# Kernel tuning notes

Measured on AMD Instinct MI355X. Metric: run time of the kernel, lower is better.

## Reference

```python
import jax, jax.numpy as jnp
import numpy as np
import math

IN_DIM = 256
HID_DIM = 256
NUM_EDGE_TYPES = 3
HEADS = 8
HEAD_DIM = HID_DIM // HEADS  # 32
QK_DIM = (NUM_EDGE_TYPES + 1) * HID_DIM  # 1024
N = 4096


def _glorot(key, shape):
    # torch_geometric-style glorot: uniform(-a, a), a = sqrt(6/(fan_in+fan_out)) over last two dims
    a = math.sqrt(6.0 / (shape[-2] + shape[-1]))
    return jax.random.uniform(key, shape, jnp.float32, -a, a)


def setup_inputs() -> dict:
    key = jax.random.key(0)
    ks = jax.random.split(key, 8)
    return {
        "input_x": jax.random.normal(ks[0], (N, IN_DIM), jnp.float32),
        "pe_Q": jax.random.normal(ks[1], (N, NUM_EDGE_TYPES * HID_DIM), jnp.float32),
        "pe_K": jax.random.normal(ks[2], (N, NUM_EDGE_TYPES * HID_DIM), jnp.float32),
        "A": jnp.zeros((N, N), jnp.int32),  # accepted by forward but unused
        "WQ": _glorot(ks[3], (HEADS, QK_DIM, HEAD_DIM)),
        "WK": _glorot(ks[4], (HEADS, QK_DIM, HEAD_DIM)),
        "WV": _glorot(ks[5], (HEADS, IN_DIM, HEAD_DIM)),
        "Q_bias": jnp.zeros((HEADS, 1, HEAD_DIM), jnp.float32),
        "K_bias": jnp.zeros((HEADS, 1, HEAD_DIM), jnp.float32),
        "V_bias": jnp.zeros((HEADS, 1, HEAD_DIM), jnp.float32),
        "lin_w": _glorot(ks[6], (HID_DIM, HID_DIM)),
        "lin_b": jnp.zeros((HID_DIM,), jnp.float32),
    }


def reference(input_x, pe_Q, pe_K, A, WQ, WK, WV, Q_bias, K_bias, V_bias, lin_w, lin_b):
    x_Q = jnp.concatenate([input_x, pe_Q], axis=-1)  # [N, QK_DIM]
    x_K = jnp.concatenate([input_x, pe_K], axis=-1)  # [N, QK_DIM]
    Q = jnp.einsum('nd,hdk->hnk', x_Q, WQ) + Q_bias   # [H, N, hd]
    K = jnp.einsum('nd,hdk->hnk', x_K, WK) + K_bias   # [H, N, hd]
    V = jnp.einsum('nd,hdk->hnk', input_x, WV) + V_bias
    scores = jnp.einsum('hnk,hmk->hnm', Q, K) / math.sqrt(HID_DIM)  # [H, N, N]
    scores = scores - jax.lax.stop_gradient(jnp.max(scores, axis=-1, keepdims=True))
    attn = jax.nn.softmax(scores, axis=-1)
    attn = jnp.where(jnp.isnan(attn), jnp.zeros_like(attn), attn)
    attn_x = jnp.einsum('hnm,hmk->hnk', attn, V)      # [H, N, hd]
    # cat(list over heads, dim=1) -> [N, H*hd] with head-major column order
    x_cat = jnp.transpose(attn_x, (1, 0, 2)).reshape(attn_x.shape[1], -1)
    return x_cat @ lin_w.T + lin_b
```

## Files before the change

kernel.cpp:

```cpp
#include <hip/hip_runtime.h>
#include <hip/hip_bf16.h>

typedef __attribute__((ext_vector_type(8))) short bf16x8;
typedef __attribute__((ext_vector_type(4))) float f32x4;

#define QSCALE 0.09016844f

__device__ __forceinline__ unsigned short f2b(float f) {
    union { float f; unsigned int u; } v; v.f = f;
    unsigned int u = v.u;
    unsigned int r = (u + 0x7FFFu + ((u >> 16) & 1u)) >> 16;
    return (unsigned short)r;
}
__device__ __forceinline__ float b2f(unsigned short h) {
    union { unsigned int u; float f; } v; v.u = ((unsigned int)h) << 16;
    return v.f;
}
__device__ __forceinline__ unsigned pk2(float a, float b) {
    union { __hip_bfloat162 h; unsigned u; } c;
    c.h = __float22bfloat162_rn(make_float2(a, b));
    return c.u;
}

__global__ __launch_bounds__(256) void prep_main(
    const float* __restrict__ WQ, const float* __restrict__ WK,
    const float* __restrict__ WV, const float* __restrict__ LW,
    const float* __restrict__ Qb, const float* __restrict__ Kb,
    const float* __restrict__ Vb,
    const float* __restrict__ x, const float* __restrict__ peQ,
    const float* __restrict__ peK,
    unsigned short* __restrict__ WQt, unsigned short* __restrict__ WKt,
    unsigned short* __restrict__ WVt, unsigned short* __restrict__ LWt,
    unsigned short* __restrict__ Bq, unsigned short* __restrict__ Bk,
    unsigned short* __restrict__ Bv,
    unsigned short* __restrict__ xb, unsigned short* __restrict__ peQb,
    unsigned short* __restrict__ peKb) {
    int b = blockIdx.x, t = threadIdx.x;
    if (b < 288) {
        const float* W; unsigned short* Wt; int h, d0, D; float sc = 1.0f;
        if (b < 128)      { W = WQ; Wt = WQt; h = b >> 4;   d0 = (b & 15) * 64; D = 1024; sc = QSCALE; }
        else if (b < 256) { int bb = b - 128; W = WK; Wt = WKt; h = bb >> 4; d0 = (bb & 15) * 64; D = 1024; }
        else              { int bb = b - 256; W = WV; Wt = WVt; h = bb >> 2; d0 = (bb & 3) * 64;  D = 256; }
        __shared__ float Ts[32][65];
        int dr = t >> 2, k0 = (t & 3) * 8;
        const float* src = W + (h * D + d0 + dr) * 32 + k0;
        float4 u0 = *(const float4*)src;
        float4 u1 = *(const float4*)(src + 4);
        Ts[k0 + 0][dr] = u0.x; Ts[k0 + 1][dr] = u0.y; Ts[k0 + 2][dr] = u0.z; Ts[k0 + 3][dr] = u0.w;
        Ts[k0 + 4][dr] = u1.x; Ts[k0 + 5][dr] = u1.y; Ts[k0 + 6][dr] = u1.z; Ts[k0 + 7][dr] = u1.w;
        __syncthreads();
        int k = t >> 3, dc = (t & 7) * 8;
        union { unsigned short s[8]; uint4 v; } pk;
#pragma unroll
        for (int i = 0; i < 8; i++) pk.s[i] = f2b(Ts[k][dc + i] * sc);
        *(uint4*)(Wt + (h * 32 + k) * D + d0 + dc) = pk.v;
    } else if (b < 320) {
        int base = (b - 288) * 2048 + t * 8;
        const float* sp = LW + base;
        float4 u0 = *(const float4*)sp;
        float4 u1 = *(const float4*)(sp + 4);
        union { unsigned u[4]; uint4 v; } pk;
        pk.u[0] = pk2(u0.x, u0.y); pk.u[1] = pk2(u0.z, u0.w);
        pk.u[2] = pk2(u1.x, u1.y); pk.u[3] = pk2(u1.z, u1.w);
        *(uint4*)(LWt + base) = pk.v;
    } else if (b == 320) {
        Bq[t] = f2b(Qb[t] * QSCALE); Bk[t] = f2b(Kb[t]); Bv[t] = f2b(Vb[t]);
    } else {
        int idx = (b - 321) * 2048 + t * 8;
        const float* sp; unsigned short* dp;
        if (idx < 1048576)      { sp = x + idx;                dp = xb + idx; }
        else if (idx < 4194304) { sp = peQ + (idx - 1048576);  dp = peQb + (idx - 1048576); }
        else                    { sp = peK + (idx - 4194304);  dp = peKb + (idx - 4194304); }
        float4 u0 = *(const float4*)sp;
        float4 u1 = *(const float4*)(sp + 4);
        union { unsigned u[4]; uint4 v; } pk;
        pk.u[0] = pk2(u0.x, u0.y); pk.u[1] = pk2(u0.z, u0.w);
        pk.u[2] = pk2(u1.x, u1.y); pk.u[3] = pk2(u1.z, u1.w);
        *(uint4*)dp = pk.v;
    }
}

__global__ __launch_bounds__(256) void prep_fb(
    const float* __restrict__ WQ, const float* __restrict__ WK,
    const float* __restrict__ WV,
    const float* __restrict__ Qb, const float* __restrict__ Kb,
    const float* __restrict__ Vb,
    unsigned short* __restrict__ WQt, unsigned short* __restrict__ WKt,
    unsigned short* __restrict__ WVt,
    unsigned short* __restrict__ Bq, unsigned short* __restrict__ Bk,
    unsigned short* __restrict__ Bv) {
    int b = blockIdx.x, t = threadIdx.x;
    if (b < 288) {
        const float* W; unsigned short* Wt; int h, d0, D; float sc = 1.0f;
        if (b < 128)      { W = WQ; Wt = WQt; h = b >> 4;   d0 = (b & 15) * 64; D = 1024; sc = QSCALE; }
        else if (b < 256) { int bb = b - 128; W = WK; Wt = WKt; h = bb >> 4; d0 = (bb & 15) * 64; D = 1024; }
        else              { int bb = b - 256; W = WV; Wt = WVt; h = bb >> 2; d0 = (bb & 3) * 64;  D = 256; }
        __shared__ float Ts[32][65];
        int dr = t >> 2, k0 = (t & 3) * 8;
        const float* src = W + (h * D + d0 + dr) * 32 + k0;
        float4 u0 = *(const float4*)src;
        float4 u1 = *(const float4*)(src + 4);
        Ts[k0 + 0][dr] = u0.x; Ts[k0 + 1][dr] = u0.y; Ts[k0 + 2][dr] = u0.z; Ts[k0 + 3][dr] = u0.w;
        Ts[k0 + 4][dr] = u1.x; Ts[k0 + 5][dr] = u1.y; Ts[k0 + 6][dr] = u1.z; Ts[k0 + 7][dr] = u1.w;
        __syncthreads();
        int k = t >> 3, dc = (t & 7) * 8;
        union { unsigned short s[8]; uint4 v; } pk;
#pragma unroll
        for (int i = 0; i < 8; i++) pk.s[i] = f2b(Ts[k][dc + i] * sc);
        *(uint4*)(Wt + (h * 32 + k) * D + d0 + dc) = pk.v;
    } else {
        Bq[t] = f2b(Qb[t] * QSCALE); Bk[t] = f2b(Kb[t]); Bv[t] = f2b(Vb[t]);
    }
}

template <bool ABF16>
__global__ __launch_bounds__(256) void proj_fused(
    const void* __restrict__ xv,
    const void* __restrict__ peQv, const void* __restrict__ peKv,
    const unsigned short* __restrict__ WQt, const unsigned short* __restrict__ WKt,
    const unsigned short* __restrict__ WVt,
    const unsigned short* __restrict__ Bq, const unsigned short* __restrict__ Bk,
    const unsigned short* __restrict__ Bv,
    unsigned short* __restrict__ Qc, unsigned short* __restrict__ KV) {
    __shared__ unsigned short As[64 * 72];
    __shared__ unsigned short Bs[64 * 72];
    int bx = blockIdx.x;
    int which = bx >> 8, bb = bx & 255;
    const void* A1; const unsigned short* Bt; const unsigned short* bias; int K;
    if (which == 0)      { A1 = peQv; Bt = WQt; bias = Bq; K = 1024; }
    else if (which == 1) { A1 = peKv; Bt = WKt; bias = Bk; K = 1024; }
    else                 { A1 = peQv; Bt = WVt; bias = Bv; K = 256; }
    int mb = bb & 63, nb = bb >> 6;
    int m0 = mb * 64, n0 = nb * 64;
    int t = threadIdx.x, w = t >> 6, lane = t & 63;
    int ln = lane & 15, q8 = (lane >> 4) * 8;
    int wm = (w >> 1) * 32, wn = (w & 1) * 32;
    int sr = t >> 3, sc = (t & 7) * 8;
    f32x4 acc[2][2];
#pragma unroll
    for (int i = 0; i < 2; i++)
#pragma unroll
        for (int j = 0; j < 2; j++) acc[i][j] = (f32x4){0.f, 0.f, 0.f, 0.f};
    for (int kb = 0; kb < K; kb += 64) {
#pragma unroll
        for (int half = 0; half < 2; half++) {
            int r = sr + half * 32;
            int c = kb + sc;
            if (ABF16) {
                const unsigned short* ap = (c < 256)
                    ? ((const unsigned short*)xv + (m0 + r) * 256 + c)
                    : ((const unsigned short*)A1 + (m0 + r) * 768 + (c - 256));
                *(uint4*)&As[r * 72 + sc] = *(const uint4*)ap;
            } else {
                const float* ap = (c < 256)
                    ? ((const float*)xv + (m0 + r) * 256 + c)
                    : ((const float*)A1 + (m0 + r) * 768 + (c - 256));
                float4 u0 = *(const float4*)ap;
                float4 u1 = *(const float4*)(ap + 4);
                union { unsigned u[4]; uint4 v; } pk;
                pk.u[0] = pk2(u0.x, u0.y); pk.u[1] = pk2(u0.z, u0.w);
                pk.u[2] = pk2(u1.x, u1.y); pk.u[3] = pk2(u1.z, u1.w);
                *(uint4*)&As[r * 72 + sc] = pk.v;
            }
            *(uint4*)&Bs[r * 72 + sc] = *(const uint4*)(Bt + (n0 + r) * K + c);
        }
        __syncthreads();
#pragma unroll
        for (int ks = 0; ks < 64; ks += 32) {
            bf16x8 a[2], b[2];
#pragma unroll
            for (int i = 0; i < 2; i++) {
                a[i] = *(const bf16x8*)&As[(wm + i * 16 + ln) * 72 + ks + q8];
                b[i] = *(const bf16x8*)&Bs[(wn + i * 16 + ln) * 72 + ks + q8];
            }
#pragma unroll
            for (int i = 0; i < 2; i++)
#pragma unroll
                for (int j = 0; j < 2; j++)
                    acc[i][j] = __builtin_amdgcn_mfma_f32_16x16x32_bf16(a[i], b[j], acc[i][j], 0, 0, 0);
        }
        __syncthreads();
    }
#pragma unroll
    for (int j = 0; j < 2; j++) {
        int ncol = n0 + wn + j * 16 + ln;
        float bv = b2f(bias[ncol]);
        int h2 = ncol >> 5, din = ncol & 31;
#pragma unroll
        for (int i = 0; i < 2; i++) {
            int rbase = m0 + wm + i * 16 + ((lane >> 4) * 4);
            if (which == 0) {
#pragma unroll
                for (int r = 0; r < 4; r++)
                    Qc[(rbase + r) * 256 + ncol] = f2b(acc[i][j][r] + bv);
            } else if (which == 1) {
#pragma unroll
                for (int r = 0; r < 4; r++) {
                    int key = rbase + r;
                    int T2 = key >> 6, k6 = key & 63;
                    int kt = ((k6 >> 2) & 1) + ((k6 >> 4) & 2);
                    int ln2 = ((k6 >> 3) & 3) * 4 + (k6 & 3);
                    int addr = (h2 * 64 + T2) * 4096 + kt * 512
                             + ((din >> 3) * 16 + ln2) * 8 + (din & 7);
                    KV[addr] = f2b(acc[i][j][r] + bv);
                }
            } else {
                int key = rbase;
                int T2 = key >> 6, k6 = key & 63;
                int chunk = 4 + ((din >> 4) << 1) + ((k6 >> 5) & 1);
                int lane2 = ((k6 >> 3) & 3) * 16 + (din & 15);
                int addr = (h2 * 64 + T2) * 4096 + chunk * 512 + lane2 * 8 + (k6 & 7);
                uint2 vv;
                vv.x = pk2(acc[i][j][0] + bv, acc[i][j][1] + bv);
                vv.y = pk2(acc[i][j][2] + bv, acc[i][j][3] + bv);
                *(uint2*)(KV + addr) = vv;
            }
        }
    }
}

__global__ __launch_bounds__(256, 2) void attn_kernel(
    const unsigned short* __restrict__ Qc,
    const unsigned short* __restrict__ KV,
    unsigned short* __restrict__ Xc) {
    __shared__ unsigned short Kt[2][4096];
    int head = blockIdx.x & 7;
    int qb = blockIdx.x >> 3;
    int tid = threadIdx.x, w = tid >> 6, lane = tid & 63;
    int ln = lane & 15, quad = lane >> 4, q8 = quad * 8;
    int q0 = qb * 64;
    int qrow = q0 + w * 16 + ln;
    bf16x8 qv = *(const bf16x8*)(Qc + qrow * 256 + head * 32 + q8);
    bf16x8 ones;
#pragma unroll
    for (int i = 0; i < 8; i++) ones[i] = (short)0x3F80;
    const f32x4 z = {0.f, 0.f, 0.f, 0.f};
    f32x4 o0 = z, o1 = z, lacc = z;
    const unsigned short* panel = KV + head * 64 * 4096;
    {
        const uint4* sp = (const uint4*)panel;
        *(uint4*)&Kt[0][tid * 16] = sp[tid * 2];
        *(uint4*)&Kt[0][tid * 16 + 8] = sp[tid * 2 + 1];
    }
    __syncthreads();
#pragma unroll 1
    for (int it = 0; it < 64; ++it) {
        int cur = it & 1;
        uint4 n0, n1;
        if (it < 63) {
            const uint4* ns = (const uint4*)(panel + (it + 1) * 4096);
            n0 = ns[tid * 2]; n1 = ns[tid * 2 + 1];
        }
        const unsigned short* kb = &Kt[cur][0];
        bf16x8 k0 = *(const bf16x8*)(kb + lane * 8);
        bf16x8 k1 = *(const bf16x8*)(kb + 512 + lane * 8);
        bf16x8 k2 = *(const bf16x8*)(kb + 1024 + lane * 8);
        bf16x8 k3 = *(const bf16x8*)(kb + 1536 + lane * 8);
        bf16x8 v0 = *(const bf16x8*)(kb + 2048 + lane * 8);
        bf16x8 v1 = *(const bf16x8*)(kb + 2560 + lane * 8);
        bf16x8 v2 = *(const bf16x8*)(kb + 3072 + lane * 8);
        bf16x8 v3 = *(const bf16x8*)(kb + 3584 + lane * 8);
        f32x4 s0 = __builtin_amdgcn_mfma_f32_16x16x32_bf16(k0, qv, z, 0, 0, 0);
        f32x4 s1 = __builtin_amdgcn_mfma_f32_16x16x32_bf16(k1, qv, z, 0, 0, 0);
        f32x4 s2 = __builtin_amdgcn_mfma_f32_16x16x32_bf16(k2, qv, z, 0, 0, 0);
        f32x4 s3 = __builtin_amdgcn_mfma_f32_16x16x32_bf16(k3, qv, z, 0, 0, 0);
        float p0[4], p1[4], p2[4], p3[4];
#pragma unroll
        for (int r = 0; r < 4; r++) {
            p0[r] = __builtin_amdgcn_exp2f(s0[r]);
            p1[r] = __builtin_amdgcn_exp2f(s1[r]);
            p2[r] = __builtin_amdgcn_exp2f(s2[r]);
            p3[r] = __builtin_amdgcn_exp2f(s3[r]);
        }
        union { unsigned u[4]; bf16x8 v; } b0, b1;
        b0.u[0] = pk2(p0[0], p0[1]); b0.u[1] = pk2(p0[2], p0[3]);
        b0.u[2] = pk2(p1[0], p1[1]); b0.u[3] = pk2(p1[2], p1[3]);
        b1.u[0] = pk2(p2[0], p2[1]); b1.u[1] = pk2(p2[2], p2[3]);
        b1.u[2] = pk2(p3[0], p3[1]); b1.u[3] = pk2(p3[2], p3[3]);
        lacc = __builtin_amdgcn_mfma_f32_16x16x32_bf16(ones, b0.v, lacc, 0, 0, 0);
        lacc = __builtin_amdgcn_mfma_f32_16x16x32_bf16(ones, b1.v, lacc, 0, 0, 0);
        o0 = __builtin_amdgcn_mfma_f32_16x16x32_bf16(v0, b0.v, o0, 0, 0, 0);
        o0 = __builtin_amdgcn_mfma_f32_16x16x32_bf16(v1, b1.v, o0, 0, 0, 0);
        o1 = __builtin_amdgcn_mfma_f32_16x16x32_bf16(v2, b0.v, o1, 0, 0, 0);
        o1 = __builtin_amdgcn_mfma_f32_16x16x32_bf16(v3, b1.v, o1, 0, 0, 0);
        __syncthreads();
        if (it < 63) {
            int nxt = cur ^ 1;
            *(uint4*)&Kt[nxt][tid * 16] = n0;
            *(uint4*)&Kt[nxt][tid * 16 + 8] = n1;
        }
        __syncthreads();
    }
    float inv = 1.f / lacc[0];
    uint2 r0v, r1v;
    r0v.x = pk2(o0[0] * inv, o0[1] * inv);
    r0v.y = pk2(o0[2] * inv, o0[3] * inv);
    r1v.x = pk2(o1[0] * inv, o1[1] * inv);
    r1v.y = pk2(o1[2] * inv, o1[3] * inv);
    unsigned short* xp = Xc + qrow * 256 + head * 32 + quad * 4;
    *(uint2*)(xp) = r0v;
    *(uint2*)(xp + 16) = r1v;
}

template <bool BBF16>
__global__ __launch_bounds__(256) void gemm_out(
    const unsigned short* __restrict__ A,
    const void* __restrict__ LWv,
    const float* __restrict__ Lb,
    float* __restrict__ C) {
    __shared__ unsigned short As[64 * 72];
    __shared__ unsigned short Bs[64 * 72];
    int mb = blockIdx.x & 63, nb = blockIdx.x >> 6;
    int m0 = mb * 64, n0 = nb * 64;
    int t = threadIdx.x, w = t >> 6, lane = t & 63;
    int ln = lane & 15, q8 = (lane >> 4) * 8;
    int wm = (w >> 1) * 32, wn = (w & 1) * 32;
    int sr = t >> 3, sc = (t & 7) * 8;
    f32x4 acc[2][2];
#pragma unroll
    for (int i = 0; i < 2; i++)
#pragma unroll
        for (int j = 0; j < 2; j++) acc[i][j] = (f32x4){0.f, 0.f, 0.f, 0.f};
    for (int kb = 0; kb < 256; kb += 64) {
#pragma unroll
        for (int half = 0; half < 2; half++) {
            int r = sr + half * 32;
            int c = kb + sc;
            *(uint4*)&As[r * 72 + sc] = *(const uint4*)(A + (m0 + r) * 256 + c);
            if (BBF16) {
                *(uint4*)&Bs[r * 72 + sc] =
                    *(const uint4*)((const unsigned short*)LWv + (n0 + r) * 256 + c);
            } else {
                const float* bp = (const float*)LWv + (n0 + r) * 256 + c;
                float4 u0 = *(const float4*)bp;
                float4 u1 = *(const float4*)(bp + 4);
                union { unsigned u[4]; uint4 v; } pk;
                pk.u[0] = pk2(u0.x, u0.y); pk.u[1] = pk2(u0.z, u0.w);
                pk.u[2] = pk2(u1.x, u1.y); pk.u[3] = pk2(u1.z, u1.w);
                *(uint4*)&Bs[r * 72 + sc] = pk.v;
            }
        }
        __syncthreads();
#pragma unroll
        for (int ks = 0; ks < 64; ks += 32) {
            bf16x8 a[2], b[2];
#pragma unroll
            for (int i = 0; i < 2; i++) {
                a[i] = *(const bf16x8*)&As[(wm + i * 16 + ln) * 72 + ks + q8];
                b[i] = *(const bf16x8*)&Bs[(wn + i * 16 + ln) * 72 + ks + q8];
            }
#pragma unroll
            for (int i = 0; i < 2; i++)
#pragma unroll
                for (int j = 0; j < 2; j++)
                    acc[i][j] = __builtin_amdgcn_mfma_f32_16x16x32_bf16(a[i], b[j], acc[i][j], 0, 0, 0);
        }
        __syncthreads();
    }
#pragma unroll
    for (int j = 0; j < 2; j++) {
        int ncol = n0 + wn + j * 16 + ln;
        float bv = Lb[ncol];
#pragma unroll
        for (int i = 0; i < 2; i++) {
            int rbase = m0 + wm + i * 16 + ((lane >> 4) * 4);
#pragma unroll
            for (int r = 0; r < 4; r++)
                C[(rbase + r) * 256 + ncol] = acc[i][j][r] + bv;
        }
    }
}

extern "C" void kernel_launch(void* const* d_in, const int* in_sizes, int n_in,
                              void* d_out, int out_size, void* d_ws, size_t ws_size,
                              hipStream_t stream) {
    const float* input_x = (const float*)d_in[0];
    const float* pe_Q    = (const float*)d_in[1];
    const float* pe_K    = (const float*)d_in[2];
    const float* WQ = (const float*)d_in[4];
    const float* WK = (const float*)d_in[5];
    const float* WV = (const float*)d_in[6];
    const float* Qb = (const float*)d_in[7];
    const float* Kb = (const float*)d_in[8];
    const float* Vb = (const float*)d_in[9];
    const float* lw = (const float*)d_in[10];
    const float* lb = (const float*)d_in[11];
    float* outp = (float*)d_out;

    unsigned short* ws = (unsigned short*)d_ws;
    unsigned short* WQt = ws;
    unsigned short* WKt = WQt + 262144;
    unsigned short* WVt = WKt + 262144;
    unsigned short* LWt = WVt + 65536;
    unsigned short* Bq  = LWt + 65536;
    unsigned short* Bk  = Bq + 256;
    unsigned short* Bv  = Bk + 256;
    unsigned short* xb   = Bv + 256;
    unsigned short* peQb = xb + 1048576;
    unsigned short* peKb = peQb + 3145728;
    unsigned short* Qc   = peKb + 3145728;
    unsigned short* KVb  = Qc + 1048576;
    unsigned short* Xc   = KVb + 2097152;
    size_t need = (size_t)(Xc + 1048576 - ws) * 2;

    if (ws_size >= need) {
        prep_main<<<dim3(3905), dim3(256), 0, stream>>>(
            WQ, WK, WV, lw, Qb, Kb, Vb, input_x, pe_Q, pe_K,
            WQt, WKt, WVt, LWt, Bq, Bk, Bv, xb, peQb, peKb);
        proj_fused<true><<<dim3(768), dim3(256), 0, stream>>>(
            xb, peQb, peKb, WQt, WKt, WVt, Bq, Bk, Bv, Qc, KVb);
        attn_kernel<<<dim3(512), dim3(256), 0, stream>>>(Qc, KVb, Xc);
        gemm_out<true><<<dim3(256), dim3(256), 0, stream>>>(Xc, LWt, lb, outp);
    } else {
        unsigned short* Qc2  = Bv + 256;
        unsigned short* KV2  = Qc2 + 1048576;
        unsigned short* Xc2  = KV2 + 2097152;
        prep_fb<<<dim3(289), dim3(256), 0, stream>>>(WQ, WK, WV, Qb, Kb, Vb,
                                                     WQt, WKt, WVt, Bq, Bk, Bv);
        proj_fused<false><<<dim3(768), dim3(256), 0, stream>>>(
            input_x, pe_Q, pe_K, WQt, WKt, WVt, Bq, Bk, Bv, Qc2, KV2);
        attn_kernel<<<dim3(512), dim3(256), 0, stream>>>(Qc2, KV2, Xc2);
        gemm_out<false><<<dim3(256), dim3(256), 0, stream>>>(Xc2, lw, lb, outp);
    }
}
```

Before: 190.3 us.

## Split attention key loop across two wave groups with LDS reduction

The attention kernel now launches 512 threads per block. Two groups of four waves each process half of the 64 key/value tiles, so each wave runs 32 iterations instead of 64. The partial outputs and denominators are then combined through shared memory before normalisation. The single barrier per iteration and sched_barrier hints aim to overlap global prefetch with MFMA work. The cost is doubled LDS staging, an extra reduction step, and possible occupancy pressure from the larger blocks.

```diff
diff --git a/kernel.cpp b/kernel.cpp
--- a/kernel.cpp
+++ b/kernel.cpp
@@ -219,17 +219,20 @@
     }
 }
 
-__global__ __launch_bounds__(256, 2) void attn_kernel(
+__global__ __launch_bounds__(512, 2) void attn_kernel(
     const unsigned short* __restrict__ Qc,
     const unsigned short* __restrict__ KV,
     unsigned short* __restrict__ Xc) {
-    __shared__ unsigned short Kt[2][4096];
+    __shared__ unsigned short Kt[2][2][4096];
+    __shared__ float Osum[2][4][16][33];
+    __shared__ float Dsum[2][4][16];
     int head = blockIdx.x & 7;
     int qb = blockIdx.x >> 3;
+    int q0 = qb * 64;
     int tid = threadIdx.x, w = tid >> 6, lane = tid & 63;
     int ln = lane & 15, quad = lane >> 4, q8 = quad * 8;
-    int q0 = qb * 64;
-    int qrow = q0 + w * 16 + ln;
+    int wr = w & 3, kg = w >> 2;
+    int qrow = q0 + wr * 16 + ln;
     bf16x8 qv = *(const bf16x8*)(Qc + qrow * 256 + head * 32 + q8);
     bf16x8 ones;
 #pragma unroll
@@ -237,21 +240,28 @@
     const f32x4 z = {0.f, 0.f, 0.f, 0.f};
     f32x4 o0 = z, o1 = z, lacc = z;
     const unsigned short* panel = KV + head * 64 * 4096;
+    int sh = tid >> 8;
+    int so0 = (wr * 2 + 0) * 512 + lane * 8;
+    int so1 = (wr * 2 + 1) * 512 + lane * 8;
     {
-        const uint4* sp = (const uint4*)panel;
-        *(uint4*)&Kt[0][tid * 16] = sp[tid * 2];
-        *(uint4*)&Kt[0][tid * 16 + 8] = sp[tid * 2 + 1];
+        const unsigned short* gp = panel + (sh * 32) * 4096;
+        uint4 a = *(const uint4*)(gp + so0);
+        uint4 b = *(const uint4*)(gp + so1);
+        *(uint4*)&Kt[0][sh][so0] = a;
+        *(uint4*)&Kt[0][sh][so1] = b;
     }
     __syncthreads();
 #pragma unroll 1
-    for (int it = 0; it < 64; ++it) {
+    for (int it = 0; it < 32; ++it) {
         int cur = it & 1;
-        uint4 n0, n1;
-        if (it < 63) {
-            const uint4* ns = (const uint4*)(panel + (it + 1) * 4096);
-            n0 = ns[tid * 2]; n1 = ns[tid * 2 + 1];
-        }
-        const unsigned short* kb = &Kt[cur][0];
+        uint4 na, nb;
+        if (it < 31) {
+            const unsigned short* gp = panel + (sh * 32 + it + 1) * 4096;
+            na = *(const uint4*)(gp + so0);
+            nb = *(const uint4*)(gp + so1);
+        }
+        __builtin_amdgcn_sched_barrier(0);
+        const unsigned short* kb = &Kt[cur][kg][0];
         bf16x8 k0 = *(const bf16x8*)(kb + lane * 8);
         bf16x8 k1 = *(const bf16x8*)(kb + 512 + lane * 8);
         bf16x8 k2 = *(const bf16x8*)(kb + 1024 + lane * 8);
@@ -272,34 +282,44 @@
             p2[r] = __builtin_amdgcn_exp2f(s2[r]);
             p3[r] = __builtin_amdgcn_exp2f(s3[r]);
         }
-        union { unsigned u[4]; bf16x8 v; } b0, b1;
-        b0.u[0] = pk2(p0[0], p0[1]); b0.u[1] = pk2(p0[2], p0[3]);
-        b0.u[2] = pk2(p1[0], p1[1]); b0.u[3] = pk2(p1[2], p1[3]);
-        b1.u[0] = pk2(p2[0], p2[1]); b1.u[1] = pk2(p2[2], p2[3]);
-        b1.u[2] = pk2(p3[0], p3[1]); b1.u[3] = pk2(p3[2], p3[3]);
-        lacc = __builtin_amdgcn_mfma_f32_16x16x32_bf16(ones, b0.v, lacc, 0, 0, 0);
-        lacc = __builtin_amdgcn_mfma_f32_16x16x32_bf16(ones, b1.v, lacc, 0, 0, 0);
-        o0 = __builtin_amdgcn_mfma_f32_16x16x32_bf16(v0, b0.v, o0, 0, 0, 0);
-        o0 = __builtin_amdgcn_mfma_f32_16x16x32_bf16(v1, b1.v, o0, 0, 0, 0);
-        o1 = __builtin_amdgcn_mfma_f32_16x16x32_bf16(v2, b0.v, o1, 0, 0, 0);
-        o1 = __builtin_amdgcn_mfma_f32_16x16x32_bf16(v3, b1.v, o1, 0, 0, 0);
-        __syncthreads();
-        if (it < 63) {
+        union { unsigned u[4]; bf16x8 v; } pa, pb;
+        pa.u[0] = pk2(p0[0], p0[1]); pa.u[1] = pk2(p0[2], p0[3]);
+        pa.u[2] = pk2(p1[0], p1[1]); pa.u[3] = pk2(p1[2], p1[3]);
+        pb.u[0] = pk2(p2[0], p2[1]); pb.u[1] = pk2(p2[2], p2[3]);
+        pb.u[2] = pk2(p3[0], p3[1]); pb.u[3] = pk2(p3[2], p3[3]);
+        lacc = __builtin_amdgcn_mfma_f32_16x16x32_bf16(ones, pa.v, lacc, 0, 0, 0);
+        lacc = __builtin_amdgcn_mfma_f32_16x16x32_bf16(ones, pb.v, lacc, 0, 0, 0);
+        o0 = __builtin_amdgcn_mfma_f32_16x16x32_bf16(v0, pa.v, o0, 0, 0, 0);
+        o0 = __builtin_amdgcn_mfma_f32_16x16x32_bf16(v1, pb.v, o0, 0, 0, 0);
+        o1 = __builtin_amdgcn_mfma_f32_16x16x32_bf16(v2, pa.v, o1, 0, 0, 0);
+        o1 = __builtin_amdgcn_mfma_f32_16x16x32_bf16(v3, pb.v, o1, 0, 0, 0);
+        __builtin_amdgcn_sched_barrier(0);
+        if (it < 31) {
             int nxt = cur ^ 1;
-            *(uint4*)&Kt[nxt][tid * 16] = n0;
-            *(uint4*)&Kt[nxt][tid * 16 + 8] = n1;
-        }
-        __syncthreads();
-    }
-    float inv = 1.f / lacc[0];
-    uint2 r0v, r1v;
-    r0v.x = pk2(o0[0] * inv, o0[1] * inv);
-    r0v.y = pk2(o0[2] * inv, o0[3] * inv);
-    r1v.x = pk2(o1[0] * inv, o1[1] * inv);
-    r1v.y = pk2(o1[2] * inv, o1[3] * inv);
-    unsigned short* xp = Xc + qrow * 256 + head * 32 + quad * 4;
-    *(uint2*)(xp) = r0v;
-    *(uint2*)(xp + 16) = r1v;
+            *(uint4*)&Kt[nxt][sh][so0] = na;
+            *(uint4*)&Kt[nxt][sh][so1] = nb;
+        }
+        __syncthreads();
+    }
+#pragma unroll
+    for (int r = 0; r < 4; r++) {
+        Osum[kg][wr][ln][quad * 4 + r] = o0[r];
+        Osum[kg][wr][ln][16 + quad * 4 + r] = o1[r];
+    }
+    if (quad == 0) Dsum[kg][wr][ln] = lacc[0];
+    __syncthreads();
+    int qr = tid >> 3, d0 = (tid & 7) * 4;
+    int rw = qr >> 4, rl = qr & 15;
+    float den = Dsum[0][rw][rl] + Dsum[1][rw][rl];
+    float inv = 1.f / den;
+    float f0 = Osum[0][rw][rl][d0 + 0] + Osum[1][rw][rl][d0 + 0];
+    float f1 = Osum[0][rw][rl][d0 + 1] + Osum[1][rw][rl][d0 + 1];
+    float f2v = Osum[0][rw][rl][d0 + 2] + Osum[1][rw][rl][d0 + 2];
+    float f3 = Osum[0][rw][rl][d0 + 3] + Osum[1][rw][rl][d0 + 3];
+    uint2 outv;
+    outv.x = pk2(f0 * inv, f1 * inv);
+    outv.y = pk2(f2v * inv, f3 * inv);
+    *(uint2*)(Xc + (q0 + qr) * 256 + head * 32 + d0) = outv;
 }
 
 template <bool BBF16>
@@ -409,7 +429,7 @@
             WQt, WKt, WVt, LWt, Bq, Bk, Bv, xb, peQb, peKb);
         proj_fused<true><<<dim3(768), dim3(256), 0, stream>>>(
             xb, peQb, peKb, WQt, WKt, WVt, Bq, Bk, Bv, Qc, KVb);
-        attn_kernel<<<dim3(512), dim3(256), 0, stream>>>(Qc, KVb, Xc);
+        attn_kernel<<<dim3(512), dim3(512), 0, stream>>>(Qc, KVb, Xc);
         gemm_out<true><<<dim3(256), dim3(256), 0, stream>>>(Xc, LWt, lb, outp);
     } else {
         unsigned short* Qc2  = Bv + 256;
@@ -419,7 +439,7 @@
                                                      WQt, WKt, WVt, Bq, Bk, Bv);
         proj_fused<false><<<dim3(768), dim3(256), 0, stream>>>(
             input_x, pe_Q, pe_K, WQt, WKt, WVt, Bq, Bk, Bv, Qc2, KV2);
-        attn_kernel<<<dim3(512), dim3(256), 0, stream>>>(Qc2, KV2, Xc2);
+        attn_kernel<<<dim3(512), dim3(512), 0, stream>>>(Qc2, KV2, Xc2);
         gemm_out<false><<<dim3(256), dim3(256), 0, stream>>>(Xc2, lw, lb, outp);
     }
 }
```

New measurement: 175.1 us, median of 2. 8.0% less time.
